# Kernel optimization log

Measured on AMD Instinct MI355X. Metric: run time of the kernel, lower is better.

The kernel has to match this reference:

```python
import jax, jax.numpy as jnp
import numpy as np

N_NODES = 50000
IN_CH = 256
HID_CH = 64
N_EDGES = 800000


def setup_inputs() -> dict:
    key = jax.random.key(0)
    k1, k2, k3, k4, k5 = jax.random.split(key, 5)
    x = jax.random.normal(k1, (N_NODES, IN_CH), dtype=jnp.float32)
    edge_index = jax.random.randint(k2, (2, N_EDGES), 0, N_NODES, dtype=jnp.int64)
    # GCNConv linear weight (Glorot) and zero bias, as in PyG defaults
    W = jax.random.normal(k3, (IN_CH, HID_CH), dtype=jnp.float32) * (1.0 / np.sqrt(IN_CH))
    bias = jnp.zeros((HID_CH,), dtype=jnp.float32)
    # PReLU per-channel weight, torch default init 0.25
    prelu_a = jnp.full((HID_CH,), 0.25, dtype=jnp.float32)
    return {"x": x, "edge_index": edge_index, "W": W, "bias": bias, "prelu_a": prelu_a}


def reference(x, edge_index, W, bias, prelu_a):
    # GCNConv, normalize=False: transform then scatter-add over edges, + bias
    xw = x @ W                               # [N, H]
    src, dst = edge_index[0], edge_index[1]
    msgs = xw[src]                           # [E, H] gather
    agg = jax.ops.segment_sum(msgs, dst, num_segments=N_NODES)  # [N, H]
    out = agg + bias
    # per-channel PReLU
    return jnp.where(out > 0, out, prelu_a * out)
```

## Files before the change

kernel.cpp:

```cpp
#include <hip/hip_runtime.h>

#define N_NODES 50000
#define IN_CH   256
#define HID_CH  64
#define N_EDGES 800000

#define AG_ROWS 64
#define NBUCKET 782
#define CAPB    1536
#define PTILE   4096
#define CAP     2048

typedef __attribute__((ext_vector_type(8))) short short8;
typedef __attribute__((ext_vector_type(4))) float f32x4;

static __device__ __forceinline__ unsigned short f2bf(float f) {
    unsigned int u = __float_as_uint(f);
    u += 0x7FFF + ((u >> 16) & 1);
    return (unsigned short)(u >> 16);
}
static __device__ __forceinline__ float bf2f(unsigned short h) {
    return __uint_as_float(((unsigned int)h) << 16);
}

__global__ __launch_bounds__(256) void wfrag_kernel(const float* __restrict__ W,
                                                    unsigned short* __restrict__ wfrag) {
    const int idx = blockIdx.x * 256 + threadIdx.x;
    if (idx >= 2048) return;
    const int ks = idx >> 8;
    const int nt = (idx >> 6) & 3;
    const int l  = idx & 63;
    const int q = l >> 4, m = l & 15;
    const int n = nt * 16 + m;
    const int k0 = ks * 32 + q * 8;
    short8 v;
    #pragma unroll
    for (int j = 0; j < 8; ++j) v[j] = (short)f2bf(W[(k0 + j) * HID_CH + n]);
    ((short8*)wfrag)[idx] = v;
}

__global__ __launch_bounds__(256) void gemm_kernel(const float* __restrict__ x,
                                                   const unsigned short* __restrict__ wfrag,
                                                   unsigned short* __restrict__ xwb) {
    const int wave = threadIdx.x >> 6;
    const int lane = threadIdx.x & 63;
    const int q = lane >> 4, m = lane & 15;
    const int row0 = blockIdx.x * 64 + wave * 16;
    const int arow = row0 + m;
    const int arl = arow < N_NODES ? arow : N_NODES - 1;
    const float* xr = x + (size_t)arl * IN_CH + q * 8;
    const short8* wf = (const short8*)wfrag;

    f32x4 acc0 = {0.f,0.f,0.f,0.f}, acc1 = acc0, acc2 = acc0, acc3 = acc0;

    #pragma unroll
    for (int ks = 0; ks < 8; ++ks) {
        const float4 a0 = *(const float4*)(xr + ks * 32);
        const float4 a1 = *(const float4*)(xr + ks * 32 + 4);
        short8 af;
        af[0] = (short)f2bf(a0.x); af[1] = (short)f2bf(a0.y);
        af[2] = (short)f2bf(a0.z); af[3] = (short)f2bf(a0.w);
        af[4] = (short)f2bf(a1.x); af[5] = (short)f2bf(a1.y);
        af[6] = (short)f2bf(a1.z); af[7] = (short)f2bf(a1.w);
        const short8 b0 = wf[(ks * 4 + 0) * 64 + lane];
        const short8 b1 = wf[(ks * 4 + 1) * 64 + lane];
        const short8 b2 = wf[(ks * 4 + 2) * 64 + lane];
        const short8 b3 = wf[(ks * 4 + 3) * 64 + lane];
        acc0 = __builtin_amdgcn_mfma_f32_16x16x32_bf16(af, b0, acc0, 0, 0, 0);
        acc1 = __builtin_amdgcn_mfma_f32_16x16x32_bf16(af, b1, acc1, 0, 0, 0);
        acc2 = __builtin_amdgcn_mfma_f32_16x16x32_bf16(af, b2, acc2, 0, 0, 0);
        acc3 = __builtin_amdgcn_mfma_f32_16x16x32_bf16(af, b3, acc3, 0, 0, 0);
    }

    #pragma unroll
    for (int r = 0; r < 4; ++r) {
        const int row = row0 + q * 4 + r;
        if (row < N_NODES) {
            unsigned short* o = xwb + (size_t)row * HID_CH + m;
            o[0]  = f2bf(acc0[r]);
            o[16] = f2bf(acc1[r]);
            o[32] = f2bf(acc2[r]);
            o[48] = f2bf(acc3[r]);
        }
    }
}

__global__ __launch_bounds__(1024) void partition_kernel(const int* __restrict__ ei,
                                                         int* __restrict__ cnt,
                                                         unsigned int* __restrict__ packed_out) {
    __shared__ int hcnt[1024];
    __shared__ int excl[1024];
    __shared__ int lcur[1024];
    __shared__ int gbase[1024];
    __shared__ unsigned int staged[PTILE];
    __shared__ unsigned short sbkt[PTILE];

    const int t = threadIdx.x;
    const int tile0 = blockIdx.x * PTILE;
    const int tcnt = min(PTILE, N_EDGES - tile0);

    hcnt[t] = 0;
    __syncthreads();

    int es[4], ed[4];
    #pragma unroll
    for (int i = 0; i < 4; ++i) {
        const int e = tile0 + t + i * 1024;
        if (e < N_EDGES) {
            es[i] = ei[e];
            ed[i] = ei[N_EDGES + e];
            atomicAdd(&hcnt[ed[i] >> 6], 1);
        } else es[i] = -1;
    }
    __syncthreads();

    const int v = hcnt[t];
    excl[t] = v;
    __syncthreads();
    for (int off = 1; off < 1024; off <<= 1) {
        const int a = excl[t];
        const int add = (t >= off) ? excl[t - off] : 0;
        __syncthreads();
        excl[t] = a + add;
        __syncthreads();
    }
    const int ex = excl[t] - v;
    __syncthreads();
    excl[t] = ex;
    lcur[t] = ex;
    if (t < NBUCKET && v > 0) gbase[t] = t * CAPB + atomicAdd(&cnt[t], v);
    __syncthreads();

    #pragma unroll
    for (int i = 0; i < 4; ++i) {
        if (es[i] >= 0) {
            const int b = ed[i] >> 6;
            const int pos = atomicAdd(&lcur[b], 1);
            staged[pos] = ((unsigned int)(ed[i] & 63) << 16) | (unsigned int)es[i];
            sbkt[pos] = (unsigned short)b;
        }
    }
    __syncthreads();

    #pragma unroll
    for (int i = 0; i < 4; ++i) {
        const int idx = t + i * 1024;
        if (idx < tcnt) {
            const int b = sbkt[idx];
            packed_out[gbase[b] + (idx - excl[b])] = staged[idx];
        }
    }
}

__global__ __launch_bounds__(512) void aggregate_kernel(const unsigned short* __restrict__ xwb,
                                                        const unsigned int* __restrict__ packed,
                                                        const int* __restrict__ cnt,
                                                        const float* __restrict__ bias,
                                                        const float* __restrict__ prelu_a,
                                                        float* __restrict__ out) {
    __shared__ unsigned int   sp[CAP];
    __shared__ unsigned short ssrc[CAP];
    __shared__ int hcnt[AG_ROWS];
    __shared__ int hexcl[AG_ROWS];
    __shared__ int hcur[AG_ROWS];
    __shared__ float acc[AG_ROWS * HID_CH];

    const int b = blockIdx.x;
    const int t = threadIdx.x;
    const int beg = b * CAPB;
    const int total = cnt[b];
    const int wv = t >> 6, lane = t & 63;
    const int slot = lane >> 4, c0 = (lane & 15) * 4;

    #pragma unroll
    for (int i = 0; i < 8; ++i) acc[t + i * 512] = 0.f;

    for (int cbeg = 0; cbeg < total; cbeg += CAP) {
        const int csz = min(CAP, total - cbeg);

        if (t < AG_ROWS) hcnt[t] = 0;
        __syncthreads();

        for (int i = t; i < csz; i += 512) {
            const unsigned int p = packed[beg + cbeg + i];
            sp[i] = p;
            atomicAdd(&hcnt[p >> 16], 1);
        }
        __syncthreads();

        if (t < AG_ROWS) hexcl[t] = hcnt[t];
        __syncthreads();
        for (int off = 1; off < AG_ROWS; off <<= 1) {
            int nv = 0;
            if (t < AG_ROWS) { nv = hexcl[t]; if (t >= off) nv += hexcl[t - off]; }
            __syncthreads();
            if (t < AG_ROWS) hexcl[t] = nv;
            __syncthreads();
        }
        if (t < AG_ROWS) { const int e = hexcl[t] - hcnt[t]; hexcl[t] = e; hcur[t] = e; }
        __syncthreads();

        for (int i = t; i < csz; i += 512) {
            const unsigned int p = sp[i];
            const int pos = atomicAdd(&hcur[p >> 16], 1);
            ssrc[pos] = (unsigned short)(p & 0xFFFFu);
        }
        __syncthreads();

        #pragma unroll
        for (int k = 0; k < 8; ++k) {
            const int nl = wv * 8 + k;
            const int rb = hexcl[nl];
            const int re = rb + hcnt[nl];
            float4 a4 = make_float4(0.f, 0.f, 0.f, 0.f);
            float4 b4 = make_float4(0.f, 0.f, 0.f, 0.f);
            int i = rb + slot;
            for (; i + 4 < re; i += 8) {
                const int s0 = ssrc[i];
                const int s1 = ssrc[i + 4];
                const ushort4 v0 = *(const ushort4*)(xwb + (size_t)s0 * HID_CH + c0);
                const ushort4 v1 = *(const ushort4*)(xwb + (size_t)s1 * HID_CH + c0);
                a4.x += bf2f(v0.x); a4.y += bf2f(v0.y);
                a4.z += bf2f(v0.z); a4.w += bf2f(v0.w);
                b4.x += bf2f(v1.x); b4.y += bf2f(v1.y);
                b4.z += bf2f(v1.z); b4.w += bf2f(v1.w);
            }
            if (i < re) {
                const int s = ssrc[i];
                const ushort4 v = *(const ushort4*)(xwb + (size_t)s * HID_CH + c0);
                a4.x += bf2f(v.x); a4.y += bf2f(v.y);
                a4.z += bf2f(v.z); a4.w += bf2f(v.w);
            }
            a4.x += b4.x; a4.y += b4.y; a4.z += b4.z; a4.w += b4.w;
            a4.x += __shfl_xor(a4.x, 16, 64); a4.y += __shfl_xor(a4.y, 16, 64);
            a4.z += __shfl_xor(a4.z, 16, 64); a4.w += __shfl_xor(a4.w, 16, 64);
            a4.x += __shfl_xor(a4.x, 32, 64); a4.y += __shfl_xor(a4.y, 32, 64);
            a4.z += __shfl_xor(a4.z, 32, 64); a4.w += __shfl_xor(a4.w, 32, 64);
            if (slot == 0) {
                float4* ap = (float4*)&acc[nl * HID_CH + c0];
                float4 c4 = *ap;
                c4.x += a4.x; c4.y += a4.y; c4.z += a4.z; c4.w += a4.w;
                *ap = c4;
            }
        }
        __syncthreads();
    }

    const int node0 = b * AG_ROWS;
    const int nrows = min(AG_ROWS, N_NODES - node0);
    for (int i = t; i < nrows * (HID_CH / 4); i += 512) {
        const int r = i >> 4;
        const int cc = (i & 15) * 4;
        const float4 a4 = *(float4*)&acc[r * HID_CH + cc];
        const float4 bb = *(const float4*)(bias + cc);
        const float4 aa = *(const float4*)(prelu_a + cc);
        float4 rr;
        rr.x = a4.x + bb.x; rr.x = rr.x > 0.f ? rr.x : aa.x * rr.x;
        rr.y = a4.y + bb.y; rr.y = rr.y > 0.f ? rr.y : aa.y * rr.y;
        rr.z = a4.z + bb.z; rr.z = rr.z > 0.f ? rr.z : aa.z * rr.z;
        rr.w = a4.w + bb.w; rr.w = rr.w > 0.f ? rr.w : aa.w * rr.w;
        *(float4*)(out + (size_t)(node0 + r) * HID_CH + cc) = rr;
    }
}

extern "C" void kernel_launch(void* const* d_in, const int* in_sizes, int n_in,
                              void* d_out, int out_size, void* d_ws, size_t ws_size,
                              hipStream_t stream) {
    const float* x       = (const float*)d_in[0];
    const int*   ei      = (const int*)d_in[1];
    const float* W       = (const float*)d_in[2];
    const float* bias    = (const float*)d_in[3];
    const float* prelu_a = (const float*)d_in[4];
    float* out = (float*)d_out;

    char* w = (char*)d_ws;
    unsigned short* xwb    = (unsigned short*)(w);
    int*            cnt    = (int*)(w + 6400000);
    unsigned int*   packed = (unsigned int*)(w + 6403200);
    unsigned short* wfrag  = (unsigned short*)(w + 11207808);

    wfrag_kernel<<<8, 256, 0, stream>>>(W, wfrag);

    gemm_kernel<<<(N_NODES + 63) / 64, 256, 0, stream>>>(x, wfrag, xwb);

    hipMemsetAsync(cnt, 0, NBUCKET * sizeof(int), stream);

    partition_kernel<<<(N_EDGES + PTILE - 1) / PTILE, 1024, 0, stream>>>(ei, cnt, packed);

    aggregate_kernel<<<NBUCKET, 512, 0, stream>>>(xwb, packed, cnt, bias, prelu_a, out);
}
```

Measured before the change: 135.9 us.

## Fuse GEMM and edge partition into one launch, drop memset and aggregate chunk loop

Merges the GEMM and partition kernels into one heterogeneous launch: the first blocks do the bf16 MFMA transform and the rest bucket edges. This lets the two independent stages overlap and saves a launch. The cnt memset moves into wfrag_kernel. The partition scan now uses wave shuffles over 782 buckets instead of a 1024-wide shared-memory Hillis-Steele scan, and the aggregate kernel drops its multi-chunk loop and unrolls the gather by four. Clamping total to CAP assumes no bucket holds more than 2048 edges, which removes the overflow path.

```diff
diff --git a/kernel.cpp b/kernel.cpp
--- a/kernel.cpp
+++ b/kernel.cpp
@@ -9,6 +9,8 @@
 #define NBUCKET 782
 #define CAPB    1536
 #define PTILE   4096
+#define NPT     196
+#define GEMM_BLOCKS 391
 #define CAP     2048
 
 typedef __attribute__((ext_vector_type(8))) short short8;
@@ -24,8 +26,10 @@
 }
 
 __global__ __launch_bounds__(256) void wfrag_kernel(const float* __restrict__ W,
-                                                    unsigned short* __restrict__ wfrag) {
+                                                    unsigned short* __restrict__ wfrag,
+                                                    int* __restrict__ cnt) {
     const int idx = blockIdx.x * 256 + threadIdx.x;
+    if (idx < NBUCKET) cnt[idx] = 0;
     if (idx >= 2048) return;
     const int ks = idx >> 8;
     const int nt = (idx >> 6) & 3;
@@ -39,73 +43,76 @@
     ((short8*)wfrag)[idx] = v;
 }
 
-__global__ __launch_bounds__(256) void gemm_kernel(const float* __restrict__ x,
-                                                   const unsigned short* __restrict__ wfrag,
-                                                   unsigned short* __restrict__ xwb) {
-    const int wave = threadIdx.x >> 6;
-    const int lane = threadIdx.x & 63;
-    const int q = lane >> 4, m = lane & 15;
-    const int row0 = blockIdx.x * 64 + wave * 16;
-    const int arow = row0 + m;
-    const int arl = arow < N_NODES ? arow : N_NODES - 1;
-    const float* xr = x + (size_t)arl * IN_CH + q * 8;
-    const short8* wf = (const short8*)wfrag;
-
-    f32x4 acc0 = {0.f,0.f,0.f,0.f}, acc1 = acc0, acc2 = acc0, acc3 = acc0;
-
-    #pragma unroll
-    for (int ks = 0; ks < 8; ++ks) {
-        const float4 a0 = *(const float4*)(xr + ks * 32);
-        const float4 a1 = *(const float4*)(xr + ks * 32 + 4);
-        short8 af;
-        af[0] = (short)f2bf(a0.x); af[1] = (short)f2bf(a0.y);
-        af[2] = (short)f2bf(a0.z); af[3] = (short)f2bf(a0.w);
-        af[4] = (short)f2bf(a1.x); af[5] = (short)f2bf(a1.y);
-        af[6] = (short)f2bf(a1.z); af[7] = (short)f2bf(a1.w);
-        const short8 b0 = wf[(ks * 4 + 0) * 64 + lane];
-        const short8 b1 = wf[(ks * 4 + 1) * 64 + lane];
-        const short8 b2 = wf[(ks * 4 + 2) * 64 + lane];
-        const short8 b3 = wf[(ks * 4 + 3) * 64 + lane];
-        acc0 = __builtin_amdgcn_mfma_f32_16x16x32_bf16(af, b0, acc0, 0, 0, 0);
-        acc1 = __builtin_amdgcn_mfma_f32_16x16x32_bf16(af, b1, acc1, 0, 0, 0);
-        acc2 = __builtin_amdgcn_mfma_f32_16x16x32_bf16(af, b2, acc2, 0, 0, 0);
-        acc3 = __builtin_amdgcn_mfma_f32_16x16x32_bf16(af, b3, acc3, 0, 0, 0);
-    }
-
-    #pragma unroll
-    for (int r = 0; r < 4; ++r) {
-        const int row = row0 + q * 4 + r;
-        if (row < N_NODES) {
-            unsigned short* o = xwb + (size_t)row * HID_CH + m;
-            o[0]  = f2bf(acc0[r]);
-            o[16] = f2bf(acc1[r]);
-            o[32] = f2bf(acc2[r]);
-            o[48] = f2bf(acc3[r]);
-        }
-    }
-}
-
-__global__ __launch_bounds__(1024) void partition_kernel(const int* __restrict__ ei,
-                                                         int* __restrict__ cnt,
-                                                         unsigned int* __restrict__ packed_out) {
-    __shared__ int hcnt[1024];
-    __shared__ int excl[1024];
-    __shared__ int lcur[1024];
-    __shared__ int gbase[1024];
+__global__ __launch_bounds__(512) void gemm_part_kernel(const float* __restrict__ x,
+                                                        const unsigned short* __restrict__ wfrag,
+                                                        unsigned short* __restrict__ xwb,
+                                                        const int* __restrict__ ei,
+                                                        int* __restrict__ cnt,
+                                                        unsigned int* __restrict__ packed_out) {
+    __shared__ int hcnt[NBUCKET];
+    __shared__ int excl[NBUCKET];
+    __shared__ int lcur[NBUCKET];
+    __shared__ int gbase[NBUCKET];
+    __shared__ int wsum[8];
     __shared__ unsigned int staged[PTILE];
     __shared__ unsigned short sbkt[PTILE];
 
     const int t = threadIdx.x;
-    const int tile0 = blockIdx.x * PTILE;
+
+    if (blockIdx.x < GEMM_BLOCKS) {
+        const int wv = t >> 6, lane = t & 63;
+        const int q = lane >> 4, m = lane & 15;
+        const int row0 = blockIdx.x * 128 + wv * 16;
+        const int arow = row0 + m;
+        const int arl = arow < N_NODES ? arow : N_NODES - 1;
+        const float* xr = x + (size_t)arl * IN_CH + q * 8;
+        const short8* wf = (const short8*)wfrag;
+
+        f32x4 acc0 = {0.f,0.f,0.f,0.f}, acc1 = acc0, acc2 = acc0, acc3 = acc0;
+
+        #pragma unroll
+        for (int ks = 0; ks < 8; ++ks) {
+            const float4 a0 = *(const float4*)(xr + ks * 32);
+            const float4 a1 = *(const float4*)(xr + ks * 32 + 4);
+            short8 af;
+            af[0] = (short)f2bf(a0.x); af[1] = (short)f2bf(a0.y);
+            af[2] = (short)f2bf(a0.z); af[3] = (short)f2bf(a0.w);
+            af[4] = (short)f2bf(a1.x); af[5] = (short)f2bf(a1.y);
+            af[6] = (short)f2bf(a1.z); af[7] = (short)f2bf(a1.w);
+            const short8 b0 = wf[(ks * 4 + 0) * 64 + lane];
+            const short8 b1 = wf[(ks * 4 + 1) * 64 + lane];
+            const short8 b2 = wf[(ks * 4 + 2) * 64 + lane];
+            const short8 b3 = wf[(ks * 4 + 3) * 64 + lane];
+            acc0 = __builtin_amdgcn_mfma_f32_16x16x32_bf16(af, b0, acc0, 0, 0, 0);
+            acc1 = __builtin_amdgcn_mfma_f32_16x16x32_bf16(af, b1, acc1, 0, 0, 0);
+            acc2 = __builtin_amdgcn_mfma_f32_16x16x32_bf16(af, b2, acc2, 0, 0, 0);
+            acc3 = __builtin_amdgcn_mfma_f32_16x16x32_bf16(af, b3, acc3, 0, 0, 0);
+        }
+
+        #pragma unroll
+        for (int r = 0; r < 4; ++r) {
+            const int row = row0 + q * 4 + r;
+            if (row < N_NODES) {
+                unsigned short* o = xwb + (size_t)row * HID_CH + m;
+                o[0]  = f2bf(acc0[r]);
+                o[16] = f2bf(acc1[r]);
+                o[32] = f2bf(acc2[r]);
+                o[48] = f2bf(acc3[r]);
+            }
+        }
+        return;
+    }
+
+    const int tile0 = (blockIdx.x - GEMM_BLOCKS) * PTILE;
     const int tcnt = min(PTILE, N_EDGES - tile0);
 
-    hcnt[t] = 0;
-    __syncthreads();
-
-    int es[4], ed[4];
-    #pragma unroll
-    for (int i = 0; i < 4; ++i) {
-        const int e = tile0 + t + i * 1024;
+    for (int i = t; i < NBUCKET; i += 512) hcnt[i] = 0;
+    __syncthreads();
+
+    int es[8], ed[8];
+    #pragma unroll
+    for (int i = 0; i < 8; ++i) {
+        const int e = tile0 + t + i * 512;
         if (e < N_EDGES) {
             es[i] = ei[e];
             ed[i] = ei[N_EDGES + e];
@@ -114,25 +121,42 @@
     }
     __syncthreads();
 
-    const int v = hcnt[t];
-    excl[t] = v;
-    __syncthreads();
-    for (int off = 1; off < 1024; off <<= 1) {
-        const int a = excl[t];
-        const int add = (t >= off) ? excl[t - off] : 0;
-        __syncthreads();
-        excl[t] = a + add;
-        __syncthreads();
-    }
-    const int ex = excl[t] - v;
-    __syncthreads();
-    excl[t] = ex;
-    lcur[t] = ex;
-    if (t < NBUCKET && v > 0) gbase[t] = t * CAPB + atomicAdd(&cnt[t], v);
-    __syncthreads();
-
-    #pragma unroll
-    for (int i = 0; i < 4; ++i) {
+    const int b0 = 2 * t, b1 = 2 * t + 1;
+    const int c0 = (b0 < NBUCKET) ? hcnt[b0] : 0;
+    const int c1 = (b1 < NBUCKET) ? hcnt[b1] : 0;
+    const int v = c0 + c1;
+    int s = v;
+    #pragma unroll
+    for (int off = 1; off < 64; off <<= 1) {
+        const int u = __shfl_up(s, off, 64);
+        if ((t & 63) >= off) s += u;
+    }
+    if ((t & 63) == 63) wsum[t >> 6] = s;
+    __syncthreads();
+    if (t < 8) {
+        const int ws = wsum[t];
+        int si = ws;
+        #pragma unroll
+        for (int off = 1; off < 8; off <<= 1) {
+            const int u = __shfl_up(si, off, 64);
+            if (t >= off) si += u;
+        }
+        wsum[t] = si - ws;
+    }
+    __syncthreads();
+    const int ex = s - v + wsum[t >> 6];
+    if (b0 < NBUCKET) {
+        excl[b0] = ex; lcur[b0] = ex;
+        if (c0 > 0) gbase[b0] = b0 * CAPB + atomicAdd(&cnt[b0], c0);
+    }
+    if (b1 < NBUCKET) {
+        excl[b1] = ex + c0; lcur[b1] = ex + c0;
+        if (c1 > 0) gbase[b1] = b1 * CAPB + atomicAdd(&cnt[b1], c1);
+    }
+    __syncthreads();
+
+    #pragma unroll
+    for (int i = 0; i < 8; ++i) {
         if (es[i] >= 0) {
             const int b = ed[i] >> 6;
             const int pos = atomicAdd(&lcur[b], 1);
@@ -143,8 +167,8 @@
     __syncthreads();
 
     #pragma unroll
-    for (int i = 0; i < 4; ++i) {
-        const int idx = t + i * 1024;
+    for (int i = 0; i < 8; ++i) {
+        const int idx = t + i * 512;
         if (idx < tcnt) {
             const int b = sbkt[idx];
             packed_out[gbase[b] + (idx - excl[b])] = staged[idx];
@@ -168,83 +192,81 @@
     const int b = blockIdx.x;
     const int t = threadIdx.x;
     const int beg = b * CAPB;
-    const int total = cnt[b];
+    const int total = min(cnt[b], CAP);
     const int wv = t >> 6, lane = t & 63;
     const int slot = lane >> 4, c0 = (lane & 15) * 4;
 
     #pragma unroll
     for (int i = 0; i < 8; ++i) acc[t + i * 512] = 0.f;
-
-    for (int cbeg = 0; cbeg < total; cbeg += CAP) {
-        const int csz = min(CAP, total - cbeg);
-
-        if (t < AG_ROWS) hcnt[t] = 0;
-        __syncthreads();
-
-        for (int i = t; i < csz; i += 512) {
-            const unsigned int p = packed[beg + cbeg + i];
-            sp[i] = p;
-            atomicAdd(&hcnt[p >> 16], 1);
-        }
-        __syncthreads();
-
-        if (t < AG_ROWS) hexcl[t] = hcnt[t];
-        __syncthreads();
-        for (int off = 1; off < AG_ROWS; off <<= 1) {
-            int nv = 0;
-            if (t < AG_ROWS) { nv = hexcl[t]; if (t >= off) nv += hexcl[t - off]; }
-            __syncthreads();
-            if (t < AG_ROWS) hexcl[t] = nv;
-            __syncthreads();
-        }
-        if (t < AG_ROWS) { const int e = hexcl[t] - hcnt[t]; hexcl[t] = e; hcur[t] = e; }
-        __syncthreads();
-
-        for (int i = t; i < csz; i += 512) {
-            const unsigned int p = sp[i];
-            const int pos = atomicAdd(&hcur[p >> 16], 1);
-            ssrc[pos] = (unsigned short)(p & 0xFFFFu);
-        }
-        __syncthreads();
-
+    if (t < AG_ROWS) hcnt[t] = 0;
+    __syncthreads();
+
+    for (int i = t; i < total; i += 512) {
+        const unsigned int p = packed[beg + i];
+        sp[i] = p;
+        atomicAdd(&hcnt[p >> 16], 1);
+    }
+    __syncthreads();
+
+    if (t < AG_ROWS) {
+        const int v = hcnt[t];
+        int s = v;
         #pragma unroll
-        for (int k = 0; k < 8; ++k) {
-            const int nl = wv * 8 + k;
-            const int rb = hexcl[nl];
-            const int re = rb + hcnt[nl];
-            float4 a4 = make_float4(0.f, 0.f, 0.f, 0.f);
-            float4 b4 = make_float4(0.f, 0.f, 0.f, 0.f);
-            int i = rb + slot;
-            for (; i + 4 < re; i += 8) {
-                const int s0 = ssrc[i];
-                const int s1 = ssrc[i + 4];
-                const ushort4 v0 = *(const ushort4*)(xwb + (size_t)s0 * HID_CH + c0);
-                const ushort4 v1 = *(const ushort4*)(xwb + (size_t)s1 * HID_CH + c0);
-                a4.x += bf2f(v0.x); a4.y += bf2f(v0.y);
-                a4.z += bf2f(v0.z); a4.w += bf2f(v0.w);
-                b4.x += bf2f(v1.x); b4.y += bf2f(v1.y);
-                b4.z += bf2f(v1.z); b4.w += bf2f(v1.w);
-            }
-            if (i < re) {
-                const int s = ssrc[i];
-                const ushort4 v = *(const ushort4*)(xwb + (size_t)s * HID_CH + c0);
-                a4.x += bf2f(v.x); a4.y += bf2f(v.y);
-                a4.z += bf2f(v.z); a4.w += bf2f(v.w);
-            }
-            a4.x += b4.x; a4.y += b4.y; a4.z += b4.z; a4.w += b4.w;
-            a4.x += __shfl_xor(a4.x, 16, 64); a4.y += __shfl_xor(a4.y, 16, 64);
-            a4.z += __shfl_xor(a4.z, 16, 64); a4.w += __shfl_xor(a4.w, 16, 64);
-            a4.x += __shfl_xor(a4.x, 32, 64); a4.y += __shfl_xor(a4.y, 32, 64);
-            a4.z += __shfl_xor(a4.z, 32, 64); a4.w += __shfl_xor(a4.w, 32, 64);
-            if (slot == 0) {
-                float4* ap = (float4*)&acc[nl * HID_CH + c0];
-                float4 c4 = *ap;
-                c4.x += a4.x; c4.y += a4.y; c4.z += a4.z; c4.w += a4.w;
-                *ap = c4;
-            }
-        }
-        __syncthreads();
-    }
+        for (int off = 1; off < 64; off <<= 1) {
+            const int u = __shfl_up(s, off, 64);
+            if (t >= off) s += u;
+        }
+        hexcl[t] = s - v;
+        hcur[t]  = s - v;
+    }
+    __syncthreads();
+
+    for (int i = t; i < total; i += 512) {
+        const unsigned int p = sp[i];
+        const int pos = atomicAdd(&hcur[p >> 16], 1);
+        ssrc[pos] = (unsigned short)(p & 0xFFFFu);
+    }
+    __syncthreads();
+
+    #pragma unroll
+    for (int k = 0; k < 8; ++k) {
+        const int nl = wv * 8 + k;
+        const int rb = hexcl[nl];
+        const int re = rb + hcnt[nl];
+        float4 a4 = make_float4(0.f, 0.f, 0.f, 0.f);
+        int i = rb + slot;
+        for (; i + 12 < re; i += 16) {
+            const int s0 = ssrc[i];
+            const int s1 = ssrc[i + 4];
+            const int s2 = ssrc[i + 8];
+            const int s3 = ssrc[i + 12];
+            const ushort4 v0 = *(const ushort4*)(xwb + (size_t)s0 * HID_CH + c0);
+            const ushort4 v1 = *(const ushort4*)(xwb + (size_t)s1 * HID_CH + c0);
+            const ushort4 v2 = *(const ushort4*)(xwb + (size_t)s2 * HID_CH + c0);
+            const ushort4 v3 = *(const ushort4*)(xwb + (size_t)s3 * HID_CH + c0);
+            a4.x += bf2f(v0.x) + bf2f(v1.x) + bf2f(v2.x) + bf2f(v3.x);
+            a4.y += bf2f(v0.y) + bf2f(v1.y) + bf2f(v2.y) + bf2f(v3.y);
+            a4.z += bf2f(v0.z) + bf2f(v1.z) + bf2f(v2.z) + bf2f(v3.z);
+            a4.w += bf2f(v0.w) + bf2f(v1.w) + bf2f(v2.w) + bf2f(v3.w);
+        }
+        for (; i < re; i += 4) {
+            const int s = ssrc[i];
+            const ushort4 v = *(const ushort4*)(xwb + (size_t)s * HID_CH + c0);
+            a4.x += bf2f(v.x); a4.y += bf2f(v.y);
+            a4.z += bf2f(v.z); a4.w += bf2f(v.w);
+        }
+        a4.x += __shfl_xor(a4.x, 16, 64); a4.y += __shfl_xor(a4.y, 16, 64);
+        a4.z += __shfl_xor(a4.z, 16, 64); a4.w += __shfl_xor(a4.w, 16, 64);
+        a4.x += __shfl_xor(a4.x, 32, 64); a4.y += __shfl_xor(a4.y, 32, 64);
+        a4.z += __shfl_xor(a4.z, 32, 64); a4.w += __shfl_xor(a4.w, 32, 64);
+        if (slot == 0) {
+            float4* ap = (float4*)&acc[nl * HID_CH + c0];
+            float4 c4 = *ap;
+            c4.x += a4.x; c4.y += a4.y; c4.z += a4.z; c4.w += a4.w;
+            *ap = c4;
+        }
+    }
+    __syncthreads();
 
     const int node0 = b * AG_ROWS;
     const int nrows = min(AG_ROWS, N_NODES - node0);
@@ -279,13 +301,9 @@
     unsigned int*   packed = (unsigned int*)(w + 6403200);
     unsigned short* wfrag  = (unsigned short*)(w + 11207808);
 
-    wfrag_kernel<<<8, 256, 0, stream>>>(W, wfrag);
-
-    gemm_kernel<<<(N_NODES + 63) / 64, 256, 0, stream>>>(x, wfrag, xwb);
-
-    hipMemsetAsync(cnt, 0, NBUCKET * sizeof(int), stream);
-
-    partition_kernel<<<(N_EDGES + PTILE - 1) / PTILE, 1024, 0, stream>>>(ei, cnt, packed);
+    wfrag_kernel<<<8, 256, 0, stream>>>(W, wfrag, cnt);
+
+    gemm_part_kernel<<<GEMM_BLOCKS + NPT, 512, 0, stream>>>(x, wfrag, xwb, ei, cnt, packed);
 
     aggregate_kernel<<<NBUCKET, 512, 0, stream>>>(xwb, packed, cnt, bias, prelu_a, out);
 }
```

New measurement: 130.7 us. 3.8% less time.
